# Optimization experiments

Measured on AMD Instinct MI355X. Metric: run time of the kernel, lower is better.

## Reference

```python
import jax, jax.numpy as jnp
import numpy as np

N_SAMPLES = 32768
CHANNELS = 128
N_ATOMS = 512
ATOM_SIZE = 512
N_TRANSFERS = 64
TRANSFER_SIZE = 8192
N_EVENTS = 32
N_ROOMS = 8
DILATIONS = (1, 3, 9, 27, 1)
BATCH = 8


def _conv1d(x, w, padding, dil=1):
    # x: [B,C,T], w: [O,I,K]
    return jax.lax.conv_general_dilated(
        x, w, (1,), padding, rhs_dilation=(dil,),
        dimension_numbers=('NCH', 'OIH', 'NCH'))


def _fft_convolve(a, b):
    # linear convolution along last dim, truncated to original length
    n = a.shape[-1]
    af = jnp.fft.rfft(a, n=2 * n)
    bf = jnp.fft.rfft(b, n=2 * n)
    return jnp.fft.irfft(af * bf, n=2 * n)[..., :n]


def _mlp(x, hw, hb, ow, ob):
    # LinearOutputStack: 3 hidden Linear(C,C)+leaky_relu, then Linear(C,out)
    for i in range(hw.shape[0]):
        x = jax.nn.leaky_relu(x @ hw[i] + hb[i], 0.2)
    return x @ ow + ob


def setup_inputs() -> dict:
    key = jax.random.key(0)
    ks = jax.random.split(key, 25)
    s = 0.02
    C = CHANNELS
    return {
        'x': jax.random.normal(ks[0], (BATCH, 1, N_SAMPLES), jnp.float32),
        'bank': jax.random.normal(ks[1], (C, 1, 512), jnp.float32) * s,
        'w_net': jax.random.normal(ks[2], (len(DILATIONS), C, C, 3), jnp.float32) * s,
        'b_net': jnp.zeros((len(DILATIONS), C), jnp.float32),
        'attn_w': jax.random.normal(ks[3], (1, C, 1), jnp.float32) * s,
        'attn_b': jnp.zeros((1,), jnp.float32),
        'atoms_hw': jax.random.normal(ks[4], (3, C, C), jnp.float32) * s,
        'atoms_hb': jnp.zeros((3, C), jnp.float32),
        'atoms_ow': jax.random.normal(ks[5], (C, N_ATOMS), jnp.float32) * s,
        'atoms_ob': jnp.zeros((N_ATOMS,), jnp.float32),
        'trans_hw': jax.random.normal(ks[6], (3, C, C), jnp.float32) * s,
        'trans_hb': jnp.zeros((3, C), jnp.float32),
        'trans_ow': jax.random.normal(ks[7], (C, N_TRANSFERS), jnp.float32) * s,
        'trans_ob': jnp.zeros((N_TRANSFERS,), jnp.float32),
        'amp_hw': jax.random.normal(ks[8], (3, C, C), jnp.float32) * s,
        'amp_hb': jnp.zeros((3, C), jnp.float32),
        'amp_ow': jax.random.normal(ks[9], (C, 1), jnp.float32) * s,
        'amp_ob': jnp.zeros((1,), jnp.float32),
        'atoms_dict': jax.random.uniform(ks[10], (N_ATOMS, ATOM_SIZE), jnp.float32, -1.0, 1.0),
        'transfer_dict': jax.random.normal(ks[11], (N_TRANSFERS, TRANSFER_SIZE), jnp.float32) * 0.01,
        'rooms': jax.random.normal(ks[12], (N_ROOMS, N_SAMPLES), jnp.float32) * 0.01,
        'room_w': jax.random.normal(ks[13], (C, N_ROOMS), jnp.float32) * s,
        'room_b': jnp.zeros((N_ROOMS,), jnp.float32),
        'mix_w': jax.random.normal(ks[14], (C, 1), jnp.float32) * s,
        'mix_b': jnp.zeros((1,), jnp.float32),
    }


def reference(x, bank, w_net, b_net, attn_w, attn_b,
              atoms_hw, atoms_hb, atoms_ow, atoms_ob,
              trans_hw, trans_hb, trans_ow, trans_ob,
              amp_hw, amp_hb, amp_ow, amp_ob,
              atoms_dict, transfer_dict, rooms, room_w, room_b, mix_w, mix_b):
    B = x.shape[0]
    # front-end filter bank, padding=256, truncate to n_samples
    h = _conv1d(x, bank, [(256, 256)])[..., :N_SAMPLES]            # [B,C,T]
    # DilatedStack: residual dilated convs
    for i, d in enumerate(DILATIONS):
        h = h + jax.nn.leaky_relu(
            _conv1d(h, w_net[i], 'SAME', d) + b_net[i][None, :, None], 0.2)
    # ExampleNorm: per-example std normalization
    h = h / (jnp.std(h, axis=(1, 2), keepdims=True) + 1e-8)
    context = jnp.max(h, axis=-1)                                   # [B,C]
    attn = jax.nn.sigmoid(_conv1d(h, attn_w, 'SAME') + attn_b[None, :, None])[:, 0, :]  # [B,T]
    # sparsify_vectors: top-k attention positions, latents scaled by attn
    vals, idx = jax.lax.top_k(attn, N_EVENTS)                        # [B,E]
    lat = jnp.take_along_axis(jnp.swapaxes(h, 1, 2), idx[..., None], axis=1) * vals[..., None]  # [B,E,C]
    atoms = jax.nn.softmax(_mlp(lat, atoms_hw, atoms_hb, atoms_ow, atoms_ob), axis=-1) @ atoms_dict
    transfers = jax.nn.softmax(_mlp(lat, trans_hw, trans_hb, trans_ow, trans_ob), axis=-1) @ transfer_dict
    amps = _mlp(lat, amp_hw, amp_hb, amp_ow, amp_ob) ** 2            # [B,E,1]
    atoms = jnp.pad(atoms, ((0, 0), (0, 0), (0, TRANSFER_SIZE - ATOM_SIZE)))
    ev = (_fft_convolve(atoms, transfers) + atoms) * amps            # [B,E,Ts]
    # overlap-add scatter. NOTE: faithful to the original, which does
    # output[:, :, idx:idx+Ts] += x[i, e] -- every event accumulates into a
    # buffer shared across the whole batch.
    pos = idx.reshape(-1)[:, None] + jnp.arange(TRANSFER_SIZE)[None, :]  # [B*E,Ts]
    buf = jnp.zeros(2 * N_SAMPLES, ev.dtype).at[pos].add(ev.reshape(-1, TRANSFER_SIZE))
    dry = jnp.broadcast_to(buf[:N_SAMPLES][None, :], (B, N_SAMPLES))  # [B,T]
    # ReverbGenerator: context -> room choice + wet/dry mix
    impulse = jax.nn.softmax(context @ room_w + room_b, axis=-1) @ rooms  # [B,T]
    mix = jax.nn.sigmoid(context @ mix_w + mix_b)                     # [B,1]
    wet = _fft_convolve(dry, impulse)
    out = dry * (1.0 - mix) + wet * mix
    return out[:, None, :]
```

## Files before the change

### kernel.cpp

```cpp
#include <hip/hip_runtime.h>
#include <math.h>

#define TSAMP 32768
#define CCH 128
#define NBATCH 8
#define NEV 32
#define NROWS 256
#define NATOMS 512
#define ASIZE 512
#define NTRANS 64
#define TSIZE 8192

#define DRY_SCALE 16777216.0f
#define IMP_SCALE 64.0f
#define WET_DESCALE 9.313225746154785e-10f

typedef _Float16 f16x8 __attribute__((ext_vector_type(8)));
typedef _Float16 f16x4 __attribute__((ext_vector_type(4)));
typedef float f32x4 __attribute__((ext_vector_type(4)));


__global__ __launch_bounds__(256) void k_zero(float* __restrict__ wet,
                                              float* __restrict__ dry,
                                              double* __restrict__ sums) {
  int i = blockIdx.x * 256 + threadIdx.x;
  if (i < NBATCH * TSAMP) wet[i] = 0.f;
  if (i < TSAMP) dry[i] = 0.f;
  if (i < 16) sums[i] = 0.0;
}

__global__ __launch_bounds__(256) void k_wsplit(const float* __restrict__ wn,
                                                _Float16* __restrict__ whi,
                                                _Float16* __restrict__ wlo) {
  const int i = blockIdx.x * 256 + threadIdx.x;
  if (i >= 245760) return;
  const int ci = i & 127;
  int r = i >> 7;
  const int o = r & 127;
  r >>= 7;
  const int k = r % 3;
  const int l = r / 3;
  const float w = wn[(((size_t)l*128 + o)*128 + ci)*3 + k];
  const _Float16 hi = (_Float16)w;
  whi[i] = hi;
  wlo[i] = (_Float16)(w - (float)hi);
}

__global__ __launch_bounds__(256) void k_bsplit(const float* __restrict__ bank,
                                                _Float16* __restrict__ bhi,
                                                _Float16* __restrict__ blo) {
  const int i = blockIdx.x * 256 + threadIdx.x;
  if (i < 65536) {
    const float w = bank[i];
    const _Float16 hi = (_Float16)w;
    bhi[i] = hi;
    blo[i] = (_Float16)(w - (float)hi);
  }
}

__global__ __launch_bounds__(256) void k_front_mfma(
    const float* __restrict__ x, const _Float16* __restrict__ bhi,
    const _Float16* __restrict__ blo, float* __restrict__ h) {
  __shared__ _Float16 shi[8*600];
  __shared__ _Float16 slo[8*600];
  const int t0 = blockIdx.x * 64;
  const int b  = blockIdx.y;
  const float* xb = x + (size_t)b*TSAMP;
  const int tid = threadIdx.x;

  for (int flat = tid; flat < 8*576; flat += 256) {
    const int p = flat / 576;
    const int q = flat - p*576;
    const int g = t0 - 256 + q + p;
    const float v = (g >= 0 && g < TSAMP) ? xb[g] : 0.f;
    const _Float16 hi = (_Float16)v;
    shi[p*600 + q] = hi;
    slo[p*600 + q] = (_Float16)(v - (float)hi);
  }
  __syncthreads();

  const int wv = tid >> 6;
  const int lane = tid & 63;
  const int n = lane & 15;
  const int quad = lane >> 4;
  const int c0 = wv * 32;
  const int ph = n & 7;
  const int nb = n & 8;

  f32x4 acc[2][4];
#pragma unroll
  for (int i = 0; i < 2; ++i)
#pragma unroll
    for (int j = 0; j < 4; ++j) acc[i][j] = (f32x4){0.f,0.f,0.f,0.f};

  for (int kc = 0; kc < 16; ++kc) {
    const int kb = kc*32 + quad*8;
    f16x8 ahi[2], alo[2];
#pragma unroll
    for (int os = 0; os < 2; ++os) {
      const size_t ao = (size_t)(c0 + os*16 + n)*512 + kb;
      ahi[os] = *(const f16x8*)(bhi + ao);
      alo[os] = *(const f16x8*)(blo + ao);
    }
    f16x8 xh[4], xl[4];
#pragma unroll
    for (int ts = 0; ts < 4; ++ts) {
      const int a = ph*600 + ts*16 + nb + kb;
      xh[ts] = *(const f16x8*)(shi + a);
      xl[ts] = *(const f16x8*)(slo + a);
    }
#pragma unroll
    for (int os = 0; os < 2; ++os)
#pragma unroll
      for (int ts = 0; ts < 4; ++ts) {
        acc[os][ts] = __builtin_amdgcn_mfma_f32_16x16x32_f16(ahi[os], xh[ts], acc[os][ts], 0, 0, 0);
        acc[os][ts] = __builtin_amdgcn_mfma_f32_16x16x32_f16(alo[os], xh[ts], acc[os][ts], 0, 0, 0);
        acc[os][ts] = __builtin_amdgcn_mfma_f32_16x16x32_f16(ahi[os], xl[ts], acc[os][ts], 0, 0, 0);
      }
  }

  float* hb = h + (size_t)b*TSAMP*CCH;
#pragma unroll
  for (int os = 0; os < 2; ++os) {
    const int cb = c0 + os*16 + quad*4;
#pragma unroll
    for (int ts = 0; ts < 4; ++ts) {
      const int t = t0 + ts*16 + n;
      *(f32x4*)(hb + (size_t)t*CCH + cb) = acc[os][ts];
    }
  }
}

__global__ __launch_bounds__(256) void k_dil_mfma(
    const float* __restrict__ hin0, const _Float16* __restrict__ whi,
    const _Float16* __restrict__ wlo, const float* __restrict__ bias,
    float* __restrict__ hout0, const int d) {
  extern __shared__ _Float16 sh[];
  const int twin = 64 + 2*d;
  _Float16* shi = sh;
  _Float16* slo = sh + twin*136;
  const int t0 = blockIdx.x * 64;
  const size_t bs = (size_t)blockIdx.y * CCH * TSAMP;
  const float* __restrict__ hin = hin0 + bs;
  float* __restrict__ hout = hout0 + bs;
  const int tid = threadIdx.x;

  for (int flat = tid; flat < twin*32; flat += 256) {
    const int tw = flat >> 5;
    const int c4 = (flat & 31) << 2;
    const int g = t0 - d + tw;
    float4 v = {0.f, 0.f, 0.f, 0.f};
    if (g >= 0 && g < TSAMP) v = *(const float4*)(hin + (size_t)g*CCH + c4);
    f16x4 hv, lv;
    hv[0] = (_Float16)v.x; hv[1] = (_Float16)v.y;
    hv[2] = (_Float16)v.z; hv[3] = (_Float16)v.w;
    lv[0] = (_Float16)(v.x - (float)hv[0]); lv[1] = (_Float16)(v.y - (float)hv[1]);
    lv[2] = (_Float16)(v.z - (float)hv[2]); lv[3] = (_Float16)(v.w - (float)hv[3]);
    *(f16x4*)(shi + tw*136 + c4) = hv;
    *(f16x4*)(slo + tw*136 + c4) = lv;
  }
  __syncthreads();

  const int wv = tid >> 6;
  const int lane = tid & 63;
  const int n = lane & 15;
  const int quad = lane >> 4;
  const int o0 = wv * 32;

  f32x4 acc[2][4];
#pragma unroll
  for (int i = 0; i < 2; ++i)
#pragma unroll
    for (int j = 0; j < 4; ++j) acc[i][j] = (f32x4){0.f,0.f,0.f,0.f};

  for (int k = 0; k < 3; ++k) {
    for (int kc = 0; kc < 4; ++kc) {
      const int cib = kc*32 + quad*8;
      f16x8 ahi[2], alo[2];
#pragma unroll
      for (int os = 0; os < 2; ++os) {
        const size_t wo = ((size_t)k*128 + (o0 + os*16 + n))*128 + cib;
        ahi[os] = *(const f16x8*)(whi + wo);
        alo[os] = *(const f16x8*)(wlo + wo);
      }
      f16x8 bhi[4], blo[4];
#pragma unroll
      for (int ts = 0; ts < 4; ++ts) {
        const int a = (ts*16 + n + k*d)*136 + cib;
        bhi[ts] = *(const f16x8*)(shi + a);
        blo[ts] = *(const f16x8*)(slo + a);
      }
#pragma unroll
      for (int os = 0; os < 2; ++os)
#pragma unroll
        for (int ts = 0; ts < 4; ++ts) {
          acc[os][ts] = __builtin_amdgcn_mfma_f32_16x16x32_f16(ahi[os], bhi[ts], acc[os][ts], 0, 0, 0);
          acc[os][ts] = __builtin_amdgcn_mfma_f32_16x16x32_f16(alo[os], bhi[ts], acc[os][ts], 0, 0, 0);
          acc[os][ts] = __builtin_amdgcn_mfma_f32_16x16x32_f16(ahi[os], blo[ts], acc[os][ts], 0, 0, 0);
        }
    }
  }

#pragma unroll
  for (int os = 0; os < 2; ++os) {
    const int ob = o0 + os*16 + quad*4;
    const f32x4 bs4 = *(const f32x4*)(bias + ob);
#pragma unroll
    for (int ts = 0; ts < 4; ++ts) {
      const int t = t0 + ts*16 + n;
      const size_t gi = (size_t)t*CCH + ob;
      const f32x4 prev = *(const f32x4*)(hin + gi);
      f32x4 res;
#pragma unroll
      for (int r = 0; r < 4; ++r) {
        float v = acc[os][ts][r] + bs4[r];
        v = v > 0.f ? v : 0.2f*v;
        res[r] = prev[r] + v;
      }
      *(f32x4*)(hout + gi) = res;
    }
  }
}

__global__ __launch_bounds__(256) void k_fuse(const float* __restrict__ h,
                                              const float* __restrict__ aw,
                                              double* __restrict__ sums,
                                              float* __restrict__ attnraw,
                                              float* __restrict__ pm) {
  const int b = blockIdx.y, slice = blockIdx.x;
  const int tid = threadIdx.x;
  const int lane = tid & 31;
  const int sub = tid >> 5;
  const float4 aw4 = *(const float4*)(aw + lane*4);
  const float* hb = h + ((size_t)b*TSAMP + (size_t)slice*512)*CCH;
  double s = 0.0, s2 = 0.0;
  float c0=-3.4e38f, c1=-3.4e38f, c2=-3.4e38f, c3=-3.4e38f;
  for (int r = 0; r < 64; ++r) {
    const int t = sub*64 + r;
    const float4 v = *(const float4*)(hb + (size_t)t*CCH + lane*4);
    s  += (double)v.x + (double)v.y + (double)v.z + (double)v.w;
    s2 += (double)v.x*v.x + (double)v.y*v.y + (double)v.z*v.z + (double)v.w*v.w;
    c0 = fmaxf(c0, v.x); c1 = fmaxf(c1, v.y);
    c2 = fmaxf(c2, v.z); c3 = fmaxf(c3, v.w);
    float dot = v.x*aw4.x + v.y*aw4.y + v.z*aw4.z + v.w*aw4.w;
    for (int sft = 16; sft; sft >>= 1) dot += __shfl_down(dot, sft, 32);
    if (lane == 0) attnraw[(size_t)b*TSAMP + slice*512 + t] = dot;
  }
  __shared__ float cl[8*128];
  cl[sub*128 + lane*4 + 0] = c0; cl[sub*128 + lane*4 + 1] = c1;
  cl[sub*128 + lane*4 + 2] = c2; cl[sub*128 + lane*4 + 3] = c3;
  __syncthreads();
  if (tid < 128) {
    float m = cl[tid];
    for (int ss = 1; ss < 8; ++ss) m = fmaxf(m, cl[ss*128 + tid]);
    pm[((size_t)b*64 + slice)*128 + tid] = m;
  }
  for (int sft = 32; sft; sft >>= 1) { s += __shfl_down(s, sft); s2 += __shfl_down(s2, sft); }
  __shared__ double sred[8];
  if ((tid & 63) == 0) { sred[(tid>>6)*2] = s; sred[(tid>>6)*2 + 1] = s2; }
  __syncthreads();
  if (tid == 0) {
    atomicAdd(&sums[b*2],     sred[0]+sred[2]+sred[4]+sred[6]);
    atomicAdd(&sums[b*2+1],   sred[1]+sred[3]+sred[5]+sred[7]);
  }
}

__global__ void k_scale(const double* __restrict__ sums, float* __restrict__ scal) {
  const int b = threadIdx.x;
  if (b < NBATCH) {
    const double n = (double)CCH * (double)TSAMP;
    const double mean = sums[b*2] / n;
    double var = sums[b*2+1] / n - mean*mean;
    if (var < 0.0) var = 0.0;
    scal[b] = (float)(1.0 / (sqrt(var) + 1e-8));
  }
}

__global__ void k_context2(const float* __restrict__ pm, const float* __restrict__ scal,
                           float* __restrict__ ctx) {
  const int b = blockIdx.x;
  const int c = threadIdx.x;
  float m = -3.4e38f;
  for (int s = 0; s < 64; ++s) m = fmaxf(m, pm[((size_t)b*64 + s)*128 + c]);
  ctx[b*128 + c] = m * scal[b];
}

__global__ __launch_bounds__(256) void k_attn2(const float* __restrict__ raw,
                                               const float* __restrict__ scal,
                                               const float* __restrict__ ab,
                                               float* __restrict__ attn) {
  const int b = blockIdx.y;
  const int i = blockIdx.x*1024 + threadIdx.x*4;
  const float s = scal[b], bb = ab[0];
  const float4 v = *(const float4*)(raw + (size_t)b*TSAMP + i);
  float* o = attn + (size_t)b*TSAMP + i;
  o[0] = 1.f/(1.f+expf(-(v.x*s+bb)));
  o[1] = 1.f/(1.f+expf(-(v.y*s+bb)));
  o[2] = 1.f/(1.f+expf(-(v.z*s+bb)));
  o[3] = 1.f/(1.f+expf(-(v.w*s+bb)));
}

__global__ __launch_bounds__(256) void k_topk1(const float* __restrict__ attn,
                                               float* __restrict__ cv,
                                               int* __restrict__ cidx) {
  const int ch = blockIdx.x, b = blockIdx.y;
  const float* a = attn + (size_t)b*TSAMP + ch*4096;
  __shared__ float v[4096];
  __shared__ float rv[4]; __shared__ int ri[4];
  const int tid = threadIdx.x;
  for (int i = tid; i < 4096; i += 256) v[i] = a[i];
  __syncthreads();
  for (int e = 0; e < NEV; ++e) {
    float bv = -1e30f; int bi = 0;
    for (int i = tid; i < 4096; i += 256) {
      const float x = v[i];
      if (x > bv) { bv = x; bi = i; }
    }
    for (int s = 32; s; s >>= 1) {
      const float ov = __shfl_down(bv, s); const int oi = __shfl_down(bi, s);
      if (ov > bv || (ov == bv && oi < bi)) { bv = ov; bi = oi; }
    }
    if ((tid & 63) == 0) { rv[tid >> 6] = bv; ri[tid >> 6] = bi; }
    __syncthreads();
    if (tid == 0) {
      int bb = 0;
      for (int w2 = 1; w2 < 4; ++w2)
        if (rv[w2] > rv[bb] || (rv[w2] == rv[bb] && ri[w2] < ri[bb])) bb = w2;
      cv[(b*8 + ch)*NEV + e] = rv[bb];
      cidx[(b*8 + ch)*NEV + e] = ch*4096 + ri[bb];
      v[ri[bb]] = -1e30f;
    }
    __syncthreads();
  }
}

__global__ __launch_bounds__(256) void k_topk2(const float* __restrict__ cv,
                                               const int* __restrict__ ci_,
                                               float* __restrict__ vals,
                                               int* __restrict__ idxs) {
  const int b = blockIdx.x;
  const int tid = threadIdx.x;
  float my = cv[b*256 + tid];
  int   mi = ci_[b*256 + tid];
  __shared__ float rv[4]; __shared__ int ri[4];
  __shared__ float bvs; __shared__ int bis;
  for (int e = 0; e < NEV; ++e) {
    float bv = my; int bi = mi;
    for (int s = 32; s; s >>= 1) {
      const float ov = __shfl_down(bv, s); const int oi = __shfl_down(bi, s);
      if (ov > bv || (ov == bv && oi < bi)) { bv = ov; bi = oi; }
    }
    if ((tid & 63) == 0) { rv[tid >> 6] = bv; ri[tid >> 6] = bi; }
    __syncthreads();
    if (tid == 0) {
      int bb = 0;
      for (int w2 = 1; w2 < 4; ++w2)
        if (rv[w2] > rv[bb] || (rv[w2] == rv[bb] && ri[w2] < ri[bb])) bb = w2;
      vals[b*NEV + e] = rv[bb]; idxs[b*NEV + e] = ri[bb];
      bvs = rv[bb]; bis = ri[bb];
    }
    __syncthreads();
    if (mi == bis && my == bvs) my = -1e30f;
    __syncthreads();
  }
}

__device__ __forceinline__ float blk_max128(float v, float* red) {
  const int tid = threadIdx.x;
  red[tid] = v; __syncthreads();
  for (int s = 64; s > 0; s >>= 1) {
    if (tid < s) red[tid] = fmaxf(red[tid], red[tid + s]);
    __syncthreads();
  }
  const float r = red[0]; __syncthreads();
  return r;
}
__device__ __forceinline__ float blk_sum128(float v, float* red) {
  const int tid = threadIdx.x;
  red[tid] = v; __syncthreads();
  for (int s = 64; s > 0; s >>= 1) {
    if (tid < s) red[tid] += red[tid + s];
    __syncthreads();
  }
  const float r = red[0]; __syncthreads();
  return r;
}
__device__ __forceinline__ float mlp_hidden3(float latv, const float* __restrict__ hw,
                                             const float* __restrict__ hb, float* xa) {
  const int tid = threadIdx.x;
  float cur = latv;
  for (int i = 0; i < 3; ++i) {
    xa[tid] = cur; __syncthreads();
    const float* W = hw + (size_t)i*CCH*CCH;
    float acc = hb[i*CCH + tid];
    for (int c = 0; c < CCH; ++c) acc += xa[c] * W[c*CCH + tid];
    cur = acc > 0.f ? acc : 0.2f*acc;
    __syncthreads();
  }
  return cur;
}

__global__ __launch_bounds__(128) void k_mlp(
    const float* __restrict__ h, const float* __restrict__ scal,
    const float* __restrict__ vals, const int* __restrict__ idxs,
    const float* __restrict__ a_hw, const float* __restrict__ a_hb,
    const float* __restrict__ a_ow, const float* __restrict__ a_ob,
    const float* __restrict__ t_hw, const float* __restrict__ t_hb,
    const float* __restrict__ t_ow, const float* __restrict__ t_ob,
    const float* __restrict__ m_hw, const float* __restrict__ m_hb,
    const float* __restrict__ m_ow, const float* __restrict__ m_ob,
    float* __restrict__ p_atoms, float* __restrict__ p_trans, float* __restrict__ amps) {
  const int row = blockIdx.x;
  const int b = row >> 5;
  const int tid = threadIdx.x;
  __shared__ float xa[CCH];
  __shared__ float red[CCH];
  const int t = idxs[row];
  const float latv = h[((size_t)b*TSAMP + t)*CCH + tid] * scal[b] * vals[row];

  {
    const float cur = mlp_hidden3(latv, a_hw, a_hb, xa);
    xa[tid] = cur; __syncthreads();
    float l0 = a_ob[tid], l1 = a_ob[tid+128], l2 = a_ob[tid+256], l3 = a_ob[tid+384];
    for (int c = 0; c < CCH; ++c) {
      const float xv = xa[c];
      const float* W = a_ow + (size_t)c*NATOMS + tid;
      l0 += xv*W[0]; l1 += xv*W[128]; l2 += xv*W[256]; l3 += xv*W[384];
    }
    const float mx = blk_max128(fmaxf(fmaxf(l0,l1), fmaxf(l2,l3)), red);
    const float e0 = expf(l0-mx), e1 = expf(l1-mx), e2 = expf(l2-mx), e3 = expf(l3-mx);
    const float inv = 1.f / blk_sum128(e0+e1+e2+e3, red);
    float* pa = p_atoms + (size_t)row*NATOMS;
    pa[tid] = e0*inv; pa[tid+128] = e1*inv; pa[tid+256] = e2*inv; pa[tid+384] = e3*inv;
  }
  {
    const float cur = mlp_hidden3(latv, t_hw, t_hb, xa);
    xa[tid] = cur; __syncthreads();
    float lg = -3.4e38f;
    if (tid < NTRANS) {
      float acc = t_ob[tid];
      for (int c = 0; c < CCH; ++c) acc += xa[c]*t_ow[c*NTRANS + tid];
      lg = acc;
    }
    const float mt = blk_max128(lg, red);
    const float et = (tid < NTRANS) ? expf(lg - mt) : 0.f;
    const float st = blk_sum128(et, red);
    if (tid < NTRANS) p_trans[(size_t)row*NTRANS + tid] = et/st;
  }
  {
    const float cur = mlp_hidden3(latv, m_hw, m_hb, xa);
    const float s = blk_sum128(cur * m_ow[tid], red);
    if (tid == 0) { const float v = s + m_ob[0]; amps[row] = v*v; }
  }
}

__global__ __launch_bounds__(256) void k_atoms_mm(const float* __restrict__ p_atoms,
                                                  const float* __restrict__ dict,
                                                  float* __restrict__ av) {
  const int row = blockIdx.x;
  __shared__ float p[NATOMS];
  for (int i = threadIdx.x; i < NATOMS; i += 256) p[i] = p_atoms[(size_t)row*NATOMS + i];
  __syncthreads();
  const int s0 = threadIdx.x*2;
  float a0=0, a1=0;
  for (int a = 0; a < NATOMS; ++a) {
    const float pa = p[a];
    const float2 dv = *(const float2*)(dict + (size_t)a*ASIZE + s0);
    a0 += pa*dv.x; a1 += pa*dv.y;
  }
  av[(size_t)row*ASIZE + s0] = a0; av[(size_t)row*ASIZE + s0 + 1] = a1;
}

__global__ __launch_bounds__(256) void k_trans_mm(const float* __restrict__ p_trans,
                                                   const float* __restrict__ td,
                                                   float* __restrict__ trans) {
  const int row = blockIdx.y;
  const int t = blockIdx.x*2048 + threadIdx.x*8;
  __shared__ float p[NTRANS];
  if (threadIdx.x < NTRANS) p[threadIdx.x] = p_trans[(size_t)row*NTRANS + threadIdx.x];
  __syncthreads();
  float a0=0,a1=0,a2=0,a3=0,a4=0,a5=0,a6=0,a7=0;
  for (int j = 0; j < NTRANS; ++j) {
    const float pj = p[j];
    const float4 v0 = *(const float4*)(td + (size_t)j*TSIZE + t);
    const float4 v1 = *(const float4*)(td + (size_t)j*TSIZE + t + 4);
    a0 += pj*v0.x; a1 += pj*v0.y; a2 += pj*v0.z; a3 += pj*v0.w;
    a4 += pj*v1.x; a5 += pj*v1.y; a6 += pj*v1.z; a7 += pj*v1.w;
  }
  float* o = trans + (size_t)row*TSIZE + t;
  o[0]=a0; o[1]=a1; o[2]=a2; o[3]=a3; o[4]=a4; o[5]=a5; o[6]=a6; o[7]=a7;
}

__global__ __launch_bounds__(256) void k_ev(const float* __restrict__ trans,
                                            const float* __restrict__ av,
                                            const float* __restrict__ amps,
                                            float* __restrict__ ev) {
  const int row = blockIdx.y;
  const int t0 = blockIdx.x * 1024;
  __shared__ float al[512];
  __shared__ float tw[1536];
  for (int i = threadIdx.x; i < 512; i += 256) al[i] = av[(size_t)row*ASIZE + i];
  for (int i = threadIdx.x; i < 1536; i += 256) {
    const int g = t0 - 512 + i;
    tw[i] = (g >= 0) ? trans[(size_t)row*TSIZE + g] : 0.f;
  }
  __syncthreads();
  const int base = threadIdx.x*4 + 512;
  float a0=0,a1=0,a2=0,a3=0;
  float w0=tw[base], w1=tw[base+1], w2=tw[base+2], w3=tw[base+3];
#pragma unroll 8
  for (int k = 0; k < 512; ++k) {
    const float ak = al[k];
    a0 += ak*w0; a1 += ak*w1; a2 += ak*w2; a3 += ak*w3;
    w3 = w2; w2 = w1; w1 = w0; w0 = tw[base - k - 1];
  }
  const int n = t0 + threadIdx.x*4;
  const float amp = amps[row];
  float* e = ev + (size_t)row*TSIZE + n;
  e[0] = (a0 + (n+0 < 512 ? al[n+0] : 0.f)) * amp;
  e[1] = (a1 + (n+1 < 512 ? al[n+1] : 0.f)) * amp;
  e[2] = (a2 + (n+2 < 512 ? al[n+2] : 0.f)) * amp;
  e[3] = (a3 + (n+3 < 512 ? al[n+3] : 0.f)) * amp;
}

__global__ __launch_bounds__(256) void k_dry(const float* __restrict__ ev,
                                             const int* __restrict__ idxs,
                                             float* __restrict__ dry) {
  __shared__ int sidx[32];
  const int r0 = blockIdx.y * 32;
  if (threadIdx.x < 32) sidx[threadIdx.x] = idxs[r0 + threadIdx.x];
  __syncthreads();
  const int p = blockIdx.x*512 + threadIdx.x*2;
  float a0=0,a1=0;
  for (int r = 0; r < 32; ++r) {
    const int off = p - sidx[r];
    if (off >= -1 && off < TSIZE) {
      const float* er = ev + (size_t)(r0 + r)*TSIZE;
      if ((unsigned)(off  ) < TSIZE) a0 += er[off];
      if ((unsigned)(off+1) < TSIZE) a1 += er[off+1];
    }
  }
  atomicAdd(dry + p,     a0);
  atomicAdd(dry + p + 1, a1);
}

__global__ __launch_bounds__(256) void k_drysplit(const float* __restrict__ dry,
                                                  _Float16* __restrict__ dhi,
                                                  _Float16* __restrict__ dlo) {
  const int i = blockIdx.x*256 + threadIdx.x;
  if (i < TSAMP) {
    const float v = dry[i] * DRY_SCALE;
    const _Float16 hi = (_Float16)v;
    dhi[i] = hi;
    dlo[i] = (_Float16)(v - (float)hi);
  }
}

__global__ void k_room(const float* __restrict__ ctx, const float* __restrict__ room_w,
                       const float* __restrict__ room_b, const float* __restrict__ mix_w,
                       const float* __restrict__ mix_b, float* __restrict__ roomp,
                       float* __restrict__ mix) {
  const int b = threadIdx.x >> 3;
  const int r = threadIdx.x & 7;
  float acc = room_b[r];
  for (int c = 0; c < CCH; ++c) acc += ctx[b*CCH + c] * room_w[c*8 + r];
  float m = acc;
  for (int s = 1; s < 8; s <<= 1) m = fmaxf(m, __shfl_xor(m, s, 8));
  const float e = expf(acc - m);
  float ssum = e;
  for (int s = 1; s < 8; s <<= 1) ssum += __shfl_xor(ssum, s, 8);
  roomp[b*8 + r] = e / ssum;
  if (r == 0) {
    float a = mix_b[0];
    for (int c = 0; c < CCH; ++c) a += ctx[b*CCH + c] * mix_w[c];
    mix[b] = 1.f/(1.f+expf(-a));
  }
}

__global__ __launch_bounds__(256) void k_impulse(const float* __restrict__ roomp,
                                                 const float* __restrict__ rooms,
                                                 _Float16* __restrict__ ihi,
                                                 _Float16* __restrict__ ilo) {
  const int b = blockIdx.y;
  const int t = blockIdx.x*1024 + threadIdx.x*4;
  float a0=0,a1=0,a2=0,a3=0;
  for (int r = 0; r < 8; ++r) {
    const float pr = roomp[b*8 + r];
    const float4 v = *(const float4*)(rooms + (size_t)r*TSAMP + t);
    a0 += pr*v.x; a1 += pr*v.y; a2 += pr*v.z; a3 += pr*v.w;
  }
  a0 *= IMP_SCALE; a1 *= IMP_SCALE; a2 *= IMP_SCALE; a3 *= IMP_SCALE;
  _Float16* oh = ihi + (size_t)b*TSAMP + t;
  _Float16* ol = ilo + (size_t)b*TSAMP + t;
  const _Float16 h0=(_Float16)a0, h1=(_Float16)a1, h2=(_Float16)a2, h3=(_Float16)a3;
  oh[0]=h0; oh[1]=h1; oh[2]=h2; oh[3]=h3;
  ol[0]=(_Float16)(a0-(float)h0); ol[1]=(_Float16)(a1-(float)h1);
  ol[2]=(_Float16)(a2-(float)h2); ol[3]=(_Float16)(a3-(float)h3);
}

__global__ __launch_bounds__(256) void k_wet_mfma(
    const _Float16* __restrict__ dhi, const _Float16* __restrict__ dlo,
    const _Float16* __restrict__ ihi, const _Float16* __restrict__ ilo,
    float* __restrict__ wet) {
  const int t0 = blockIdx.x * 256;
  const int k0 = blockIdx.y * 4096;
  if (k0 > t0 + 255) return;
  __shared__ _Float16 rhi[8*776];
  __shared__ _Float16 rlo[8*776];
  const int tid = threadIdx.x;
  const int wv = tid >> 6;
  const int lane = tid & 63;
  const int n16 = lane & 15;
  const int quad = lane >> 4;
  const int m = n16;

  f32x4 acc[4];
#pragma unroll
  for (int j = 0; j < 4; ++j) acc[j] = (f32x4){0.f,0.f,0.f,0.f};

  const int kend = (k0 + 4096 < t0 + 256) ? k0 + 4096 : t0 + 256;
  const int ph = 7 - (n16 & 7);
  for (int kc0 = k0; kc0 < kend; kc0 += 512) {
    const int D0 = t0 + 255 - kc0;
    for (int flat = tid; flat < 8*768; flat += 256) {
      const int p = flat / 768;
      const int q = flat - p*768;
      const int di = D0 - q - p;
      _Float16 hi = (_Float16)0.f, lo = (_Float16)0.f;
      if (di >= 0 && di < TSAMP) { hi = dhi[di]; lo = dlo[di]; }
      rhi[p*776 + q] = hi;
      rlo[p*776 + q] = lo;
    }
    __syncthreads();

#pragma unroll 4
    for (int kc = 0; kc < 16; ++kc) {
      const int kb = kc*32;
      const int jg = kc0 + kb + quad*8;
      f16x8 ah, al;
      if (m < NBATCH) {
        const size_t ao = (size_t)m*TSAMP + jg;
        ah = *(const f16x8*)(ihi + ao);
        al = *(const f16x8*)(ilo + ao);
      } else {
        ah = (f16x8){0,0,0,0,0,0,0,0};
        al = (f16x8){0,0,0,0,0,0,0,0};
      }
#pragma unroll
      for (int ts = 0; ts < 4; ++ts) {
        const int nn = wv*64 + ts*16 + n16;
        const int a = ph*776 + kb + quad*8 + 248 - (nn & ~7);
        const f16x8 bh = *(const f16x8*)(rhi + a);
        const f16x8 bl = *(const f16x8*)(rlo + a);
        acc[ts] = __builtin_amdgcn_mfma_f32_16x16x32_f16(ah, bh, acc[ts], 0, 0, 0);
        acc[ts] = __builtin_amdgcn_mfma_f32_16x16x32_f16(al, bh, acc[ts], 0, 0, 0);
        acc[ts] = __builtin_amdgcn_mfma_f32_16x16x32_f16(ah, bl, acc[ts], 0, 0, 0);
      }
    }
    __syncthreads();
  }

#pragma unroll
  for (int ts = 0; ts < 4; ++ts) {
    const int t = t0 + wv*64 + ts*16 + n16;
#pragma unroll
    for (int r = 0; r < 4; ++r) {
      const int b = quad*4 + r;
      if (b < NBATCH)
        atomicAdd(wet + (size_t)b*TSAMP + t, acc[ts][r] * WET_DESCALE);
    }
  }
}

__global__ __launch_bounds__(256) void k_out(const float* __restrict__ dry,
                                             const float* __restrict__ wet,
                                             const float* __restrict__ mix,
                                             float* __restrict__ out) {
  const int b = blockIdx.y;
  const int t = blockIdx.x*1024 + threadIdx.x*4;
  const float m = mix[b];
  const float4 d = *(const float4*)(dry + t);
  const float4 w = *(const float4*)(wet + (size_t)b*TSAMP + t);
  float* o = out + (size_t)b*TSAMP + t;
  o[0] = d.x*(1.f-m) + w.x*m;
  o[1] = d.y*(1.f-m) + w.y*m;
  o[2] = d.z*(1.f-m) + w.z*m;
  o[3] = d.w*(1.f-m) + w.w*m;
}

extern "C" void kernel_launch(void* const* d_in, const int* in_sizes, int n_in,
                              void* d_out, int out_size, void* d_ws, size_t ws_size,
                              hipStream_t stream) {
  (void)in_sizes; (void)n_in; (void)out_size; (void)ws_size;
  const float* x      = (const float*)d_in[0];
  const float* bank   = (const float*)d_in[1];
  const float* w_net  = (const float*)d_in[2];
  const float* b_net  = (const float*)d_in[3];
  const float* attn_w = (const float*)d_in[4];
  const float* attn_b = (const float*)d_in[5];
  const float* a_hw = (const float*)d_in[6];
  const float* a_hb = (const float*)d_in[7];
  const float* a_ow = (const float*)d_in[8];
  const float* a_ob = (const float*)d_in[9];
  const float* t_hw = (const float*)d_in[10];
  const float* t_hb = (const float*)d_in[11];
  const float* t_ow = (const float*)d_in[12];
  const float* t_ob = (const float*)d_in[13];
  const float* m_hw = (const float*)d_in[14];
  const float* m_hb = (const float*)d_in[15];
  const float* m_ow = (const float*)d_in[16];
  const float* m_ob = (const float*)d_in[17];
  const float* atoms_dict    = (const float*)d_in[18];
  const float* transfer_dict = (const float*)d_in[19];
  const float* rooms  = (const float*)d_in[20];
  const float* room_w = (const float*)d_in[21];
  const float* room_b = (const float*)d_in[22];
  const float* mix_w  = (const float*)d_in[23];
  const float* mix_b  = (const float*)d_in[24];
  float* out = (float*)d_out;

  float* ws = (float*)d_ws;
  float* H  = ws;
  float* t1 = ws + (size_t)33554432;
  float* t2 = ws + (size_t)41943040;
  _Float16* whi = (_Float16*)(ws + (size_t)50331648);
  _Float16* wlo = (_Float16*)(ws + (size_t)50454528);
  _Float16* bhi = (_Float16*)(ws + (size_t)50577408);
  _Float16* blo = (_Float16*)(ws + (size_t)50610176);

  size_t off = 33554432;
  double* sums = (double*)(ws + off); off += 32;
  float* attn  = ws + off; off += (size_t)NBATCH*TSAMP;
  float* attnraw = ws + off; off += (size_t)NBATCH*TSAMP;
  float* pm    = ws + off; off += (size_t)NBATCH*64*CCH;
  float* scal  = ws + off; off += 8;
  float* ctx   = ws + off; off += NBATCH*CCH;
  float* vals  = ws + off; off += NROWS;
  int*   idxs  = (int*)(ws + off); off += NROWS;
  float* p_atoms = ws + off; off += (size_t)NROWS*NATOMS;
  float* p_trans = ws + off; off += (size_t)NROWS*NTRANS;
  float* amps  = ws + off; off += NROWS;
  float* av    = ws + off; off += (size_t)NROWS*ASIZE;
  float* trans = ws + off; off += (size_t)NROWS*TSIZE;
  float* ev    = ws + off; off += (size_t)NROWS*TSIZE;
  float* dry   = ws + off; off += TSAMP;
  float* roomp = ws + off; off += 64;
  float* mix   = ws + off; off += 8;
  float* wet   = ws + off; off += (size_t)NBATCH*TSAMP;
  float* cand_v = ws + off; off += 2048;
  int*   cand_i = (int*)(ws + off); off += 2048;
  _Float16* imphi = (_Float16*)(ws + off); off += (size_t)NBATCH*TSAMP/2;
  _Float16* implo = (_Float16*)(ws + off); off += (size_t)NBATCH*TSAMP/2;
  _Float16* dryhi = (_Float16*)(ws + off); off += TSAMP/2;
  _Float16* drylo = (_Float16*)(ws + off); off += TSAMP/2;

  k_wsplit<<<960, 256, 0, stream>>>(w_net, whi, wlo);
  k_bsplit<<<256, 256, 0, stream>>>(bank, bhi, blo);
  k_front_mfma<<<dim3(512, 8), 256, 0, stream>>>(x, bhi, blo, H);

  const int dil[5] = {1, 3, 9, 27, 1};
  const size_t S = (size_t)CCH * TSAMP;
  for (int p = 0; p < 4; ++p) {
    float* Hp = H + (size_t)(2*p) * S;
    float* io[6] = {Hp, t1, t2, t1, t2, Hp};
    for (int i = 0; i < 5; ++i) {
      const int d = dil[i];
      const size_t smem = (size_t)(64 + 2*d) * 544;
      k_dil_mfma<<<dim3(512, 2), 256, smem, stream>>>(
          io[i], whi + (size_t)i*49152, wlo + (size_t)i*49152, b_net + i*CCH,
          io[i+1], d);
    }
  }

  k_zero<<<1024, 256, 0, stream>>>(wet, dry, sums);
  k_fuse<<<dim3(64, 8), 256, 0, stream>>>(H, attn_w, sums, attnraw, pm);
  k_scale<<<1, 64, 0, stream>>>(sums, scal);
  k_context2<<<8, 128, 0, stream>>>(pm, scal, ctx);
  k_attn2<<<dim3(32, 8), 256, 0, stream>>>(attnraw, scal, attn_b, attn);
  k_topk1<<<dim3(8, 8), 256, 0, stream>>>(attn, cand_v, cand_i);
  k_topk2<<<8, 256, 0, stream>>>(cand_v, cand_i, vals, idxs);
  k_mlp<<<256, 128, 0, stream>>>(H, scal, vals, idxs,
                                 a_hw, a_hb, a_ow, a_ob,
                                 t_hw, t_hb, t_ow, t_ob,
                                 m_hw, m_hb, m_ow, m_ob,
                                 p_atoms, p_trans, amps);
  k_atoms_mm<<<256, 256, 0, stream>>>(p_atoms, atoms_dict, av);
  k_trans_mm<<<dim3(4, 256), 256, 0, stream>>>(p_trans, transfer_dict, trans);
  k_ev<<<dim3(8, 256), 256, 0, stream>>>(trans, av, amps, ev);
  k_dry<<<dim3(64, 8), 256, 0, stream>>>(ev, idxs, dry);
  k_drysplit<<<128, 256, 0, stream>>>(dry, dryhi, drylo);
  k_room<<<1, 64, 0, stream>>>(ctx, room_w, room_b, mix_w, mix_b, roomp, mix);
  k_impulse<<<dim3(32, 8), 256, 0, stream>>>(roomp, rooms, imphi, implo);
  k_wet_mfma<<<dim3(128, 8), 256, 0, stream>>>(dryhi, drylo, imphi, implo, wet);
  k_out<<<dim3(32, 8), 256, 0, stream>>>(dry, wet, mix, out);
}
```

Before: 1.483 ms.

## Fuse attention stats into last dilated conv, drop split-fp16 for wet conv, retile front

The per-time reduction that computed sums, attention logits and channel maxima moves into a new epilogue on the final dilated-conv layer, which removes a separate full pass over the hidden tensor. The dilated conv residual is now read from the already staged fp16 hi/lo shared tile instead of being reloaded from global memory. The reverb convolution drops the hi/lo split and runs a single fp16 MFMA on a pre-reversed dry signal with larger output tiles, which cuts its MFMA count and loads but lowers accuracy. The front conv tile doubles to 128 time steps per block so the bank weights are reused more. The max partials grow to 512 per batch, so the context reduction loop gets longer.

```diff
diff --git a/kernel.cpp b/kernel.cpp
--- a/kernel.cpp
+++ b/kernel.cpp
@@ -20,13 +20,15 @@
 typedef float f32x4 __attribute__((ext_vector_type(4)));
 
 
+__global__ void k_zs(double* __restrict__ sums) {
+  if (threadIdx.x < 16) sums[threadIdx.x] = 0.0;
+}
+
 __global__ __launch_bounds__(256) void k_zero(float* __restrict__ wet,
-                                              float* __restrict__ dry,
-                                              double* __restrict__ sums) {
+                                              float* __restrict__ dry) {
   int i = blockIdx.x * 256 + threadIdx.x;
   if (i < NBATCH * TSAMP) wet[i] = 0.f;
   if (i < TSAMP) dry[i] = 0.f;
-  if (i < 16) sums[i] = 0.0;
 }
 
 __global__ __launch_bounds__(256) void k_wsplit(const float* __restrict__ wn,
@@ -61,21 +63,21 @@
 __global__ __launch_bounds__(256) void k_front_mfma(
     const float* __restrict__ x, const _Float16* __restrict__ bhi,
     const _Float16* __restrict__ blo, float* __restrict__ h) {
-  __shared__ _Float16 shi[8*600];
-  __shared__ _Float16 slo[8*600];
-  const int t0 = blockIdx.x * 64;
+  __shared__ _Float16 shi[8*664];
+  __shared__ _Float16 slo[8*664];
+  const int t0 = blockIdx.x * 128;
   const int b  = blockIdx.y;
   const float* xb = x + (size_t)b*TSAMP;
   const int tid = threadIdx.x;
 
-  for (int flat = tid; flat < 8*576; flat += 256) {
-    const int p = flat / 576;
-    const int q = flat - p*576;
+  for (int flat = tid; flat < 8*632; flat += 256) {
+    const int p = flat / 632;
+    const int q = flat - p*632;
     const int g = t0 - 256 + q + p;
     const float v = (g >= 0 && g < TSAMP) ? xb[g] : 0.f;
     const _Float16 hi = (_Float16)v;
-    shi[p*600 + q] = hi;
-    slo[p*600 + q] = (_Float16)(v - (float)hi);
+    shi[p*664 + q] = hi;
+    slo[p*664 + q] = (_Float16)(v - (float)hi);
   }
   __syncthreads();
 
@@ -87,11 +89,11 @@
   const int ph = n & 7;
   const int nb = n & 8;
 
-  f32x4 acc[2][4];
+  f32x4 acc[2][8];
 #pragma unroll
   for (int i = 0; i < 2; ++i)
 #pragma unroll
-    for (int j = 0; j < 4; ++j) acc[i][j] = (f32x4){0.f,0.f,0.f,0.f};
+    for (int j = 0; j < 8; ++j) acc[i][j] = (f32x4){0.f,0.f,0.f,0.f};
 
   for (int kc = 0; kc < 16; ++kc) {
     const int kb = kc*32 + quad*8;
@@ -102,21 +104,26 @@
       ahi[os] = *(const f16x8*)(bhi + ao);
       alo[os] = *(const f16x8*)(blo + ao);
     }
-    f16x8 xh[4], xl[4];
-#pragma unroll
-    for (int ts = 0; ts < 4; ++ts) {
-      const int a = ph*600 + ts*16 + nb + kb;
-      xh[ts] = *(const f16x8*)(shi + a);
-      xl[ts] = *(const f16x8*)(slo + a);
-    }
-#pragma unroll
-    for (int os = 0; os < 2; ++os)
-#pragma unroll
-      for (int ts = 0; ts < 4; ++ts) {
-        acc[os][ts] = __builtin_amdgcn_mfma_f32_16x16x32_f16(ahi[os], xh[ts], acc[os][ts], 0, 0, 0);
-        acc[os][ts] = __builtin_amdgcn_mfma_f32_16x16x32_f16(alo[os], xh[ts], acc[os][ts], 0, 0, 0);
-        acc[os][ts] = __builtin_amdgcn_mfma_f32_16x16x32_f16(ahi[os], xl[ts], acc[os][ts], 0, 0, 0);
+#pragma unroll
+    for (int tg = 0; tg < 2; ++tg) {
+      f16x8 xh[4], xl[4];
+#pragma unroll
+      for (int u = 0; u < 4; ++u) {
+        const int a = ph*664 + (tg*4 + u)*16 + nb + kb;
+        xh[u] = *(const f16x8*)(shi + a);
+        xl[u] = *(const f16x8*)(slo + a);
       }
+#pragma unroll
+      for (int os = 0; os < 2; ++os)
+#pragma unroll
+        for (int u = 0; u < 4; ++u) {
+          f32x4 a4 = acc[os][tg*4 + u];
+          a4 = __builtin_amdgcn_mfma_f32_16x16x32_f16(ahi[os], xh[u], a4, 0, 0, 0);
+          a4 = __builtin_amdgcn_mfma_f32_16x16x32_f16(alo[os], xh[u], a4, 0, 0, 0);
+          a4 = __builtin_amdgcn_mfma_f32_16x16x32_f16(ahi[os], xl[u], a4, 0, 0, 0);
+          acc[os][tg*4 + u] = a4;
+        }
+    }
   }
 
   float* hb = h + (size_t)b*TSAMP*CCH;
@@ -124,7 +131,7 @@
   for (int os = 0; os < 2; ++os) {
     const int cb = c0 + os*16 + quad*4;
 #pragma unroll
-    for (int ts = 0; ts < 4; ++ts) {
+    for (int ts = 0; ts < 8; ++ts) {
       const int t = t0 + ts*16 + n;
       *(f32x4*)(hb + (size_t)t*CCH + cb) = acc[os][ts];
     }
@@ -208,60 +215,162 @@
 #pragma unroll
     for (int ts = 0; ts < 4; ++ts) {
       const int t = t0 + ts*16 + n;
-      const size_t gi = (size_t)t*CCH + ob;
-      const f32x4 prev = *(const f32x4*)(hin + gi);
+      const int tw = ts*16 + n + d;
+      const f16x4 phv = *(const f16x4*)(shi + tw*136 + ob);
+      const f16x4 plv = *(const f16x4*)(slo + tw*136 + ob);
       f32x4 res;
 #pragma unroll
       for (int r = 0; r < 4; ++r) {
         float v = acc[os][ts][r] + bs4[r];
         v = v > 0.f ? v : 0.2f*v;
-        res[r] = prev[r] + v;
+        res[r] = (float)phv[r] + (float)plv[r] + v;
       }
-      *(f32x4*)(hout + gi) = res;
-    }
-  }
-}
-
-__global__ __launch_bounds__(256) void k_fuse(const float* __restrict__ h,
-                                              const float* __restrict__ aw,
-                                              double* __restrict__ sums,
-                                              float* __restrict__ attnraw,
-                                              float* __restrict__ pm) {
-  const int b = blockIdx.y, slice = blockIdx.x;
-  const int tid = threadIdx.x;
-  const int lane = tid & 31;
-  const int sub = tid >> 5;
-  const float4 aw4 = *(const float4*)(aw + lane*4);
-  const float* hb = h + ((size_t)b*TSAMP + (size_t)slice*512)*CCH;
+      *(f32x4*)(hout + (size_t)t*CCH + ob) = res;
+    }
+  }
+}
+
+__global__ __launch_bounds__(256) void k_dil_last(
+    const float* __restrict__ hin0, const _Float16* __restrict__ whi,
+    const _Float16* __restrict__ wlo, const float* __restrict__ bias,
+    float* __restrict__ hout0, const int d,
+    const float* __restrict__ aw, double* __restrict__ sums,
+    float* __restrict__ attnraw, float* __restrict__ pm, const int bb0) {
+  extern __shared__ _Float16 sh[];
+  const int twin = 64 + 2*d;
+  _Float16* shi = sh;
+  _Float16* slo = sh + twin*136;
+  __shared__ float attl[4*64];
+  __shared__ double sred[8];
+  const int t0 = blockIdx.x * 64;
+  const int b = bb0 + blockIdx.y;
+  const size_t bs = (size_t)blockIdx.y * CCH * TSAMP;
+  const float* __restrict__ hin = hin0 + bs;
+  float* __restrict__ hout = hout0 + bs;
+  const int tid = threadIdx.x;
+
+  for (int flat = tid; flat < twin*32; flat += 256) {
+    const int tw = flat >> 5;
+    const int c4 = (flat & 31) << 2;
+    const int g = t0 - d + tw;
+    float4 v = {0.f, 0.f, 0.f, 0.f};
+    if (g >= 0 && g < TSAMP) v = *(const float4*)(hin + (size_t)g*CCH + c4);
+    f16x4 hv, lv;
+    hv[0] = (_Float16)v.x; hv[1] = (_Float16)v.y;
+    hv[2] = (_Float16)v.z; hv[3] = (_Float16)v.w;
+    lv[0] = (_Float16)(v.x - (float)hv[0]); lv[1] = (_Float16)(v.y - (float)hv[1]);
+    lv[2] = (_Float16)(v.z - (float)hv[2]); lv[3] = (_Float16)(v.w - (float)hv[3]);
+    *(f16x4*)(shi + tw*136 + c4) = hv;
+    *(f16x4*)(slo + tw*136 + c4) = lv;
+  }
+  __syncthreads();
+
+  const int wv = tid >> 6;
+  const int lane = tid & 63;
+  const int n = lane & 15;
+  const int quad = lane >> 4;
+  const int o0 = wv * 32;
+
+  f32x4 acc[2][4];
+#pragma unroll
+  for (int i = 0; i < 2; ++i)
+#pragma unroll
+    for (int j = 0; j < 4; ++j) acc[i][j] = (f32x4){0.f,0.f,0.f,0.f};
+
+  for (int k = 0; k < 3; ++k) {
+    for (int kc = 0; kc < 4; ++kc) {
+      const int cib = kc*32 + quad*8;
+      f16x8 ahi[2], alo[2];
+#pragma unroll
+      for (int os = 0; os < 2; ++os) {
+        const size_t wo = ((size_t)k*128 + (o0 + os*16 + n))*128 + cib;
+        ahi[os] = *(const f16x8*)(whi + wo);
+        alo[os] = *(const f16x8*)(wlo + wo);
+      }
+      f16x8 bhi[4], blo[4];
+#pragma unroll
+      for (int ts = 0; ts < 4; ++ts) {
+        const int a = (ts*16 + n + k*d)*136 + cib;
+        bhi[ts] = *(const f16x8*)(shi + a);
+        blo[ts] = *(const f16x8*)(slo + a);
+      }
+#pragma unroll
+      for (int os = 0; os < 2; ++os)
+#pragma unroll
+        for (int ts = 0; ts < 4; ++ts) {
+          acc[os][ts] = __builtin_amdgcn_mfma_f32_16x16x32_f16(ahi[os], bhi[ts], acc[os][ts], 0, 0, 0);
+          acc[os][ts] = __builtin_amdgcn_mfma_f32_16x16x32_f16(alo[os], bhi[ts], acc[os][ts], 0, 0, 0);
+          acc[os][ts] = __builtin_amdgcn_mfma_f32_16x16x32_f16(ahi[os], blo[ts], acc[os][ts], 0, 0, 0);
+        }
+    }
+  }
+
+  const f32x4 awq0 = *(const f32x4*)(aw + o0 + quad*4);
+  const f32x4 awq1 = *(const f32x4*)(aw + o0 + 16 + quad*4);
   double s = 0.0, s2 = 0.0;
-  float c0=-3.4e38f, c1=-3.4e38f, c2=-3.4e38f, c3=-3.4e38f;
-  for (int r = 0; r < 64; ++r) {
-    const int t = sub*64 + r;
-    const float4 v = *(const float4*)(hb + (size_t)t*CCH + lane*4);
-    s  += (double)v.x + (double)v.y + (double)v.z + (double)v.w;
-    s2 += (double)v.x*v.x + (double)v.y*v.y + (double)v.z*v.z + (double)v.w*v.w;
-    c0 = fmaxf(c0, v.x); c1 = fmaxf(c1, v.y);
-    c2 = fmaxf(c2, v.z); c3 = fmaxf(c3, v.w);
-    float dot = v.x*aw4.x + v.y*aw4.y + v.z*aw4.z + v.w*aw4.w;
-    for (int sft = 16; sft; sft >>= 1) dot += __shfl_down(dot, sft, 32);
-    if (lane == 0) attnraw[(size_t)b*TSAMP + slice*512 + t] = dot;
-  }
-  __shared__ float cl[8*128];
-  cl[sub*128 + lane*4 + 0] = c0; cl[sub*128 + lane*4 + 1] = c1;
-  cl[sub*128 + lane*4 + 2] = c2; cl[sub*128 + lane*4 + 3] = c3;
+  float pa[4] = {0.f, 0.f, 0.f, 0.f};
+  f32x4 cm[2];
+  cm[0] = (f32x4){-3.4e38f, -3.4e38f, -3.4e38f, -3.4e38f};
+  cm[1] = cm[0];
+
+#pragma unroll
+  for (int os = 0; os < 2; ++os) {
+    const int ob = o0 + os*16 + quad*4;
+    const f32x4 bs4 = *(const f32x4*)(bias + ob);
+    const f32x4 awv = os ? awq1 : awq0;
+#pragma unroll
+    for (int ts = 0; ts < 4; ++ts) {
+      const int t = t0 + ts*16 + n;
+      const int tw = ts*16 + n + d;
+      const f16x4 phv = *(const f16x4*)(shi + tw*136 + ob);
+      const f16x4 plv = *(const f16x4*)(slo + tw*136 + ob);
+      f32x4 res;
+      float dotp = 0.f;
+#pragma unroll
+      for (int r = 0; r < 4; ++r) {
+        float v = acc[os][ts][r] + bs4[r];
+        v = v > 0.f ? v : 0.2f*v;
+        const float hv = (float)phv[r] + (float)plv[r] + v;
+        res[r] = hv;
+        s += (double)hv; s2 += (double)hv*(double)hv;
+        dotp += hv * awv[r];
+        cm[os][r] = fmaxf(cm[os][r], hv);
+      }
+      pa[ts] += dotp;
+      *(f32x4*)(hout + (size_t)t*CCH + ob) = res;
+    }
+  }
+
+#pragma unroll
+  for (int ts = 0; ts < 4; ++ts) {
+    pa[ts] += __shfl_xor(pa[ts], 16);
+    pa[ts] += __shfl_xor(pa[ts], 32);
+  }
+  if (quad == 0) {
+#pragma unroll
+    for (int ts = 0; ts < 4; ++ts) attl[wv*64 + ts*16 + n] = pa[ts];
+  }
+#pragma unroll
+  for (int mk = 1; mk <= 8; mk <<= 1)
+#pragma unroll
+    for (int os = 0; os < 2; ++os)
+#pragma unroll
+      for (int r = 0; r < 4; ++r)
+        cm[os][r] = fmaxf(cm[os][r], __shfl_xor(cm[os][r], mk));
+  if (n == 0) {
+#pragma unroll
+    for (int os = 0; os < 2; ++os)
+      *(f32x4*)(pm + ((size_t)b*512 + blockIdx.x)*128 + o0 + os*16 + quad*4) = cm[os];
+  }
+  for (int sft = 32; sft; sft >>= 1) { s += __shfl_down(s, sft); s2 += __shfl_down(s2, sft); }
+  if (lane == 0) { sred[wv*2] = s; sred[wv*2+1] = s2; }
   __syncthreads();
-  if (tid < 128) {
-    float m = cl[tid];
-    for (int ss = 1; ss < 8; ++ss) m = fmaxf(m, cl[ss*128 + tid]);
-    pm[((size_t)b*64 + slice)*128 + tid] = m;
-  }
-  for (int sft = 32; sft; sft >>= 1) { s += __shfl_down(s, sft); s2 += __shfl_down(s2, sft); }
-  __shared__ double sred[8];
-  if ((tid & 63) == 0) { sred[(tid>>6)*2] = s; sred[(tid>>6)*2 + 1] = s2; }
-  __syncthreads();
+  if (tid < 64)
+    attnraw[(size_t)b*TSAMP + t0 + tid] =
+        attl[tid] + attl[64 + tid] + attl[128 + tid] + attl[192 + tid];
   if (tid == 0) {
-    atomicAdd(&sums[b*2],     sred[0]+sred[2]+sred[4]+sred[6]);
-    atomicAdd(&sums[b*2+1],   sred[1]+sred[3]+sred[5]+sred[7]);
+    atomicAdd(&sums[b*2],   sred[0] + sred[2] + sred[4] + sred[6]);
+    atomicAdd(&sums[b*2+1], sred[1] + sred[3] + sred[5] + sred[7]);
   }
 }
 
@@ -281,7 +390,7 @@
   const int b = blockIdx.x;
   const int c = threadIdx.x;
   float m = -3.4e38f;
-  for (int s = 0; s < 64; ++s) m = fmaxf(m, pm[((size_t)b*64 + s)*128 + c]);
+  for (int s = 0; s < 512; ++s) m = fmaxf(m, pm[((size_t)b*512 + s)*128 + c]);
   ctx[b*128 + c] = m * scal[b];
 }
 
@@ -544,16 +653,11 @@
   atomicAdd(dry + p + 1, a1);
 }
 
-__global__ __launch_bounds__(256) void k_drysplit(const float* __restrict__ dry,
-                                                  _Float16* __restrict__ dhi,
-                                                  _Float16* __restrict__ dlo) {
+__global__ __launch_bounds__(256) void k_dryrev(const float* __restrict__ dry,
+                                                _Float16* __restrict__ drev) {
   const int i = blockIdx.x*256 + threadIdx.x;
-  if (i < TSAMP) {
-    const float v = dry[i] * DRY_SCALE;
-    const _Float16 hi = (_Float16)v;
-    dhi[i] = hi;
-    dlo[i] = (_Float16)(v - (float)hi);
-  }
+  if (i < TSAMP + 1088)
+    drev[i] = (i < TSAMP) ? (_Float16)(dry[TSAMP-1-i] * DRY_SCALE) : (_Float16)0.f;
 }
 
 __global__ void k_room(const float* __restrict__ ctx, const float* __restrict__ room_w,
@@ -579,8 +683,7 @@
 
 __global__ __launch_bounds__(256) void k_impulse(const float* __restrict__ roomp,
                                                  const float* __restrict__ rooms,
-                                                 _Float16* __restrict__ ihi,
-                                                 _Float16* __restrict__ ilo) {
+                                                 _Float16* __restrict__ ihi) {
   const int b = blockIdx.y;
   const int t = blockIdx.x*1024 + threadIdx.x*4;
   float a0=0,a1=0,a2=0,a3=0;
@@ -589,24 +692,18 @@
     const float4 v = *(const float4*)(rooms + (size_t)r*TSAMP + t);
     a0 += pr*v.x; a1 += pr*v.y; a2 += pr*v.z; a3 += pr*v.w;
   }
-  a0 *= IMP_SCALE; a1 *= IMP_SCALE; a2 *= IMP_SCALE; a3 *= IMP_SCALE;
   _Float16* oh = ihi + (size_t)b*TSAMP + t;
-  _Float16* ol = ilo + (size_t)b*TSAMP + t;
-  const _Float16 h0=(_Float16)a0, h1=(_Float16)a1, h2=(_Float16)a2, h3=(_Float16)a3;
-  oh[0]=h0; oh[1]=h1; oh[2]=h2; oh[3]=h3;
-  ol[0]=(_Float16)(a0-(float)h0); ol[1]=(_Float16)(a1-(float)h1);
-  ol[2]=(_Float16)(a2-(float)h2); ol[3]=(_Float16)(a3-(float)h3);
+  oh[0] = (_Float16)(a0*IMP_SCALE); oh[1] = (_Float16)(a1*IMP_SCALE);
+  oh[2] = (_Float16)(a2*IMP_SCALE); oh[3] = (_Float16)(a3*IMP_SCALE);
 }
 
 __global__ __launch_bounds__(256) void k_wet_mfma(
-    const _Float16* __restrict__ dhi, const _Float16* __restrict__ dlo,
-    const _Float16* __restrict__ ihi, const _Float16* __restrict__ ilo,
+    const _Float16* __restrict__ drev, const _Float16* __restrict__ ihi,
     float* __restrict__ wet) {
-  const int t0 = blockIdx.x * 256;
+  const int t0 = blockIdx.x * 512;
   const int k0 = blockIdx.y * 4096;
-  if (k0 > t0 + 255) return;
-  __shared__ _Float16 rhi[8*776];
-  __shared__ _Float16 rlo[8*776];
+  if (k0 > t0 + 511) return;
+  __shared__ _Float16 rhi[8*1048];
   const int tid = threadIdx.x;
   const int wv = tid >> 6;
   const int lane = tid & 63;
@@ -614,22 +711,18 @@
   const int quad = lane >> 4;
   const int m = n16;
 
-  f32x4 acc[4];
-#pragma unroll
-  for (int j = 0; j < 4; ++j) acc[j] = (f32x4){0.f,0.f,0.f,0.f};
-
-  const int kend = (k0 + 4096 < t0 + 256) ? k0 + 4096 : t0 + 256;
+  f32x4 acc[8];
+#pragma unroll
+  for (int j = 0; j < 8; ++j) acc[j] = (f32x4){0.f,0.f,0.f,0.f};
+
+  const int kend = (k0 + 4096 < t0 + 512) ? k0 + 4096 : t0 + 512;
   const int ph = 7 - (n16 & 7);
   for (int kc0 = k0; kc0 < kend; kc0 += 512) {
-    const int D0 = t0 + 255 - kc0;
-    for (int flat = tid; flat < 8*768; flat += 256) {
-      const int p = flat / 768;
-      const int q = flat - p*768;
-      const int di = D0 - q - p;
-      _Float16 hi = (_Float16)0.f, lo = (_Float16)0.f;
-      if (di >= 0 && di < TSAMP) { hi = dhi[di]; lo = dlo[di]; }
-      rhi[p*776 + q] = hi;
-      rlo[p*776 + q] = lo;
+    const int RB = TSAMP - 1 - (t0 + 511 - kc0);
+    for (int flat = tid; flat < 8*1016; flat += 256) {
+      const int p = flat / 1016;
+      const int q = flat - p*1016;
+      rhi[p*1048 + q] = drev[RB + p + q];
     }
     __syncthreads();
 
@@ -637,32 +730,23 @@
     for (int kc = 0; kc < 16; ++kc) {
       const int kb = kc*32;
       const int jg = kc0 + kb + quad*8;
-      f16x8 ah, al;
-      if (m < NBATCH) {
-        const size_t ao = (size_t)m*TSAMP + jg;
-        ah = *(const f16x8*)(ihi + ao);
-        al = *(const f16x8*)(ilo + ao);
-      } else {
-        ah = (f16x8){0,0,0,0,0,0,0,0};
-        al = (f16x8){0,0,0,0,0,0,0,0};
+      f16x8 ah;
+      if (m < NBATCH) ah = *(const f16x8*)(ihi + (size_t)m*TSAMP + jg);
+      else ah = (f16x8){0,0,0,0,0,0,0,0};
+#pragma unroll
+      for (int ts = 0; ts < 8; ++ts) {
+        const int nn = wv*128 + ts*16 + n16;
+        const int a = ph*1048 + kb + quad*8 + 504 - (nn & ~7);
+        const f16x8 bh = *(const f16x8*)(rhi + a);
+        acc[ts] = __builtin_amdgcn_mfma_f32_16x16x32_f16(ah, bh, acc[ts], 0, 0, 0);
       }
-#pragma unroll
-      for (int ts = 0; ts < 4; ++ts) {
-        const int nn = wv*64 + ts*16 + n16;
-        const int a = ph*776 + kb + quad*8 + 248 - (nn & ~7);
-        const f16x8 bh = *(const f16x8*)(rhi + a);
-        const f16x8 bl = *(const f16x8*)(rlo + a);
-        acc[ts] = __builtin_amdgcn_mfma_f32_16x16x32_f16(ah, bh, acc[ts], 0, 0, 0);
-        acc[ts] = __builtin_amdgcn_mfma_f32_16x16x32_f16(al, bh, acc[ts], 0, 0, 0);
-        acc[ts] = __builtin_amdgcn_mfma_f32_16x16x32_f16(ah, bl, acc[ts], 0, 0, 0);
-      }
-    }
-    __syncthreads();
-  }
-
-#pragma unroll
-  for (int ts = 0; ts < 4; ++ts) {
-    const int t = t0 + wv*64 + ts*16 + n16;
+    }
+    __syncthreads();
+  }
+
+#pragma unroll
+  for (int ts = 0; ts < 8; ++ts) {
+    const int t = t0 + wv*128 + ts*16 + n16;
 #pragma unroll
     for (int r = 0; r < 4; ++r) {
       const int b = quad*4 + r;
@@ -727,12 +811,12 @@
   _Float16* wlo = (_Float16*)(ws + (size_t)50454528);
   _Float16* bhi = (_Float16*)(ws + (size_t)50577408);
   _Float16* blo = (_Float16*)(ws + (size_t)50610176);
+  double* sums  = (double*)(ws + (size_t)50642944);
+  float* attnraw = ws + (size_t)50642976;
+  float* pm      = ws + (size_t)50905120;
 
   size_t off = 33554432;
-  double* sums = (double*)(ws + off); off += 32;
   float* attn  = ws + off; off += (size_t)NBATCH*TSAMP;
-  float* attnraw = ws + off; off += (size_t)NBATCH*TSAMP;
-  float* pm    = ws + off; off += (size_t)NBATCH*64*CCH;
   float* scal  = ws + off; off += 8;
   float* ctx   = ws + off; off += NBATCH*CCH;
   float* vals  = ws + off; off += NROWS;
@@ -750,30 +834,35 @@
   float* cand_v = ws + off; off += 2048;
   int*   cand_i = (int*)(ws + off); off += 2048;
   _Float16* imphi = (_Float16*)(ws + off); off += (size_t)NBATCH*TSAMP/2;
-  _Float16* implo = (_Float16*)(ws + off); off += (size_t)NBATCH*TSAMP/2;
-  _Float16* dryhi = (_Float16*)(ws + off); off += TSAMP/2;
-  _Float16* drylo = (_Float16*)(ws + off); off += TSAMP/2;
-
+  _Float16* drev  = (_Float16*)(ws + off); off += (TSAMP + 1088)/2 + 4;
+
+  k_zs<<<1, 64, 0, stream>>>(sums);
   k_wsplit<<<960, 256, 0, stream>>>(w_net, whi, wlo);
   k_bsplit<<<256, 256, 0, stream>>>(bank, bhi, blo);
-  k_front_mfma<<<dim3(512, 8), 256, 0, stream>>>(x, bhi, blo, H);
+  k_front_mfma<<<dim3(256, 8), 256, 0, stream>>>(x, bhi, blo, H);
 
   const int dil[5] = {1, 3, 9, 27, 1};
   const size_t S = (size_t)CCH * TSAMP;
   for (int p = 0; p < 4; ++p) {
     float* Hp = H + (size_t)(2*p) * S;
     float* io[6] = {Hp, t1, t2, t1, t2, Hp};
-    for (int i = 0; i < 5; ++i) {
+    for (int i = 0; i < 4; ++i) {
       const int d = dil[i];
       const size_t smem = (size_t)(64 + 2*d) * 544;
       k_dil_mfma<<<dim3(512, 2), 256, smem, stream>>>(
           io[i], whi + (size_t)i*49152, wlo + (size_t)i*49152, b_net + i*CCH,
           io[i+1], d);
     }
-  }
-
-  k_zero<<<1024, 256, 0, stream>>>(wet, dry, sums);
-  k_fuse<<<dim3(64, 8), 256, 0, stream>>>(H, attn_w, sums, attnraw, pm);
+    {
+      const int d = dil[4];
+      const size_t smem = (size_t)(64 + 2*d) * 544;
+      k_dil_last<<<dim3(512, 2), 256, smem, stream>>>(
+          io[4], whi + (size_t)4*49152, wlo + (size_t)4*49152, b_net + 4*CCH,
+          io[5], d, attn_w, sums, attnraw, pm, 2*p);
+    }
+  }
+
+  k_zero<<<1024, 256, 0, stream>>>(wet, dry);
   k_scale<<<1, 64, 0, stream>>>(sums, scal);
   k_context2<<<8, 128, 0, stream>>>(pm, scal, ctx);
   k_attn2<<<dim3(32, 8), 256, 0, stream>>>(attnraw, scal, attn_b, attn);
@@ -788,9 +877,9 @@
   k_trans_mm<<<dim3(4, 256), 256, 0, stream>>>(p_trans, transfer_dict, trans);
   k_ev<<<dim3(8, 256), 256, 0, stream>>>(trans, av, amps, ev);
   k_dry<<<dim3(64, 8), 256, 0, stream>>>(ev, idxs, dry);
-  k_drysplit<<<128, 256, 0, stream>>>(dry, dryhi, drylo);
+  k_dryrev<<<133, 256, 0, stream>>>(dry, drev);
   k_room<<<1, 64, 0, stream>>>(ctx, room_w, room_b, mix_w, mix_b, roomp, mix);
-  k_impulse<<<dim3(32, 8), 256, 0, stream>>>(roomp, rooms, imphi, implo);
-  k_wet_mfma<<<dim3(128, 8), 256, 0, stream>>>(dryhi, drylo, imphi, implo, wet);
+  k_impulse<<<dim3(32, 8), 256, 0, stream>>>(roomp, rooms, imphi);
+  k_wet_mfma<<<dim3(64, 8), 256, 0, stream>>>(drev, imphi, wet);
   k_out<<<dim3(32, 8), 256, 0, stream>>>(dry, wet, mix, out);
 }
```

After: 1.472 ms. Within noise of the previous version (-0.7%).
